# Kernel optimization log

Measured on AMD Instinct MI355X. Metric: run time of the kernel, lower is better.

## Reference

```python
import jax, jax.numpy as jnp
import numpy as np

N_HEADS = 32
N_KV_HEADS = 8
HEAD_DIM = 128
DIM = 4096
BSZ = 2
SEQLEN = 2048
ROPE_THETA = 500000.0


def setup_inputs() -> dict:
    key = jax.random.key(0)
    ks = jax.random.split(key, 6)
    s = 0.02
    x = jax.random.normal(ks[0], (BSZ, SEQLEN, DIM), dtype=jnp.float32)
    wq = jax.random.normal(ks[1], (N_HEADS * HEAD_DIM, DIM), dtype=jnp.float32) * s
    wk = jax.random.normal(ks[2], (N_KV_HEADS * HEAD_DIM, DIM), dtype=jnp.float32) * s
    wv = jax.random.normal(ks[3], (N_KV_HEADS * HEAD_DIM, DIM), dtype=jnp.float32) * s
    wo = jax.random.normal(ks[4], (DIM, N_HEADS * HEAD_DIM), dtype=jnp.float32) * s
    cache_k = jnp.zeros((BSZ, SEQLEN, N_KV_HEADS, HEAD_DIM), dtype=jnp.float32)
    cache_v = jnp.zeros((BSZ, SEQLEN, N_KV_HEADS, HEAD_DIM), dtype=jnp.float32)
    # rotary frequencies: freqs_cis[t, j] = exp(i * t * theta^(-2j/hd)); pass cos/sin parts
    inv = 1.0 / (ROPE_THETA ** (jnp.arange(0, HEAD_DIM, 2, dtype=jnp.float32) / HEAD_DIM))
    t = jnp.arange(SEQLEN, dtype=jnp.float32)
    ang = jnp.outer(t, inv)  # [S, hd/2]
    freqs_cos = jnp.cos(ang)
    freqs_sin = jnp.sin(ang)
    # causal additive mask
    mask = jnp.triu(jnp.full((SEQLEN, SEQLEN), -jnp.inf, dtype=jnp.float32), k=1)
    return {"x": x, "wq": wq, "wk": wk, "wv": wv, "wo": wo,
            "cache_k": cache_k, "cache_v": cache_v,
            "freqs_cos": freqs_cos, "freqs_sin": freqs_sin,
            "mask": mask, "start_pos": 0}


def _apply_rope(t, cos, sin):
    # t: [B, S, h, hd]; cos/sin: [S, hd/2]
    B, S, h, hd = t.shape
    tf = t.astype(jnp.float32).reshape(B, S, h, hd // 2, 2)
    a, b = tf[..., 0], tf[..., 1]
    c = cos[None, :, None, :]
    s = sin[None, :, None, :]
    out = jnp.stack([a * c - b * s, a * s + b * c], axis=-1)
    return out.reshape(B, S, h, hd).astype(t.dtype)


def reference(x, wq, wk, wv, wo, cache_k, cache_v, freqs_cos, freqs_sin, mask, start_pos):
    B, S, D = x.shape
    hd = HEAD_DIM
    n_rep = N_HEADS // N_KV_HEADS
    xq = (x @ wq.T).reshape(B, S, N_HEADS, hd)
    xk = (x @ wk.T).reshape(B, S, N_KV_HEADS, hd)
    xv = (x @ wv.T).reshape(B, S, N_KV_HEADS, hd)
    xq = _apply_rope(xq, freqs_cos, freqs_sin)
    xk = _apply_rope(xk, freqs_cos, freqs_sin)
    # KV cache write + slice
    cache_k = jax.lax.dynamic_update_slice(cache_k, xk, (0, start_pos, 0, 0))
    cache_v = jax.lax.dynamic_update_slice(cache_v, xv, (0, start_pos, 0, 0))
    kv_len = start_pos + S
    keys = cache_k[:B, :kv_len]    # [B, K, kvh, hd]
    values = cache_v[:B, :kv_len]
    # GQA: repeat kv heads
    keys = jnp.repeat(keys, n_rep, axis=2)     # [B, K, H, hd]
    values = jnp.repeat(values, n_rep, axis=2)
    q = xq.transpose(0, 2, 1, 3)       # [B, H, S, hd]
    k = keys.transpose(0, 2, 1, 3)     # [B, H, K, hd]
    v = values.transpose(0, 2, 1, 3)
    scores = jnp.einsum('bhqd,bhkd->bhqk', q, k) / jnp.sqrt(jnp.float32(hd))
    if mask is not None:
        scores = scores + mask[None, None, :, :]
    probs = jax.nn.softmax(scores.astype(jnp.float32), axis=-1).astype(q.dtype)
    out = jnp.einsum('bhqk,bhkd->bhqd', probs, v)
    out = out.transpose(0, 2, 1, 3).reshape(B, S, N_HEADS * hd)
    return out @ wo.T
```

## Files before the change

kernel.cpp:

```cpp
#include <hip/hip_runtime.h>
#include <hip/hip_bf16.h>
#include <math.h>

typedef __attribute__((ext_vector_type(8)))  __bf16 bfrag;
typedef __attribute__((ext_vector_type(4)))  float  f32x4;
typedef __attribute__((ext_vector_type(16))) float  f32x16;
typedef __attribute__((ext_vector_type(8)))  short  s16x8;
typedef __attribute__((ext_vector_type(4)))  short  s16x4;
typedef __attribute__((ext_vector_type(2)))  unsigned u32x2;
typedef __attribute__((ext_vector_type(4)))  unsigned u32x4;

__device__ __forceinline__ short f2bf(float f) {
  return (short)__builtin_bit_cast(unsigned short, (__bf16)f);
}
__device__ __forceinline__ float bf2f(short s) {
  return (float)__builtin_bit_cast(__bf16, (unsigned short)s);
}
__device__ __forceinline__ unsigned cvtpk(float lo, float hi_) {
  unsigned r;
  asm("v_cvt_pk_bf16_f32 %0, %1, %2" : "=v"(r) : "v"(lo), "v"(hi_));
  return r;
}
__device__ __forceinline__ void gll16(const void* g, void* l) {
  __builtin_amdgcn_global_load_lds((const __attribute__((address_space(1))) void*)g,
                                   (__attribute__((address_space(3))) void*)l, 16, 0, 0);
}

__global__ __launch_bounds__(256) void cvt_f32_bf16(const float* __restrict__ in,
                                                    short* __restrict__ out, int n4) {
  int i = blockIdx.x * 256 + threadIdx.x;
  if (i >= n4) return;
  f32x4 v = ((const f32x4*)in)[i];
  s16x4 o;
  o.x = f2bf(v.x); o.y = f2bf(v.y); o.z = f2bf(v.z); o.w = f2bf(v.w);
  ((s16x4*)out)[i] = o;
}

__global__ __launch_bounds__(256) void cvt4(const float* __restrict__ x,
                                            const float* __restrict__ wq,
                                            const float* __restrict__ wk,
                                            const float* __restrict__ wv,
                                            short* __restrict__ xb,
                                            short* __restrict__ wqb,
                                            short* __restrict__ wkb,
                                            short* __restrict__ wvb) {
  const int b = blockIdx.x;
  const float* in; short* out; int base;
  if (b < 16384)      { in = x;  out = xb;  base = 0; }
  else if (b < 32768) { in = wq; out = wqb; base = 16384 * 256; }
  else if (b < 36864) { in = wk; out = wkb; base = 32768 * 256; }
  else                { in = wv; out = wvb; base = 36864 * 256; }
  const int idx = b * 256 + threadIdx.x - base;
  f32x4 v = ((const f32x4*)in)[idx];
  s16x4 o;
  o.x = f2bf(v.x); o.y = f2bf(v.y); o.z = f2bf(v.z); o.w = f2bf(v.w);
  ((s16x4*)out)[idx] = o;
}

template<bool BF16OUT>
__global__ __launch_bounds__(512) void gemm128n(const short* __restrict__ A,
                                                const short* __restrict__ B,
                                                void* __restrict__ Cv,
                                                int M, int N, int K, int NBX) {
  __shared__ __align__(16) short As[2][128 * 64];
  __shared__ __align__(16) short Bs[2][256 * 64];
  const int tid = threadIdx.x, lane = tid & 63, wid = tid >> 6;
  const int lr = lane & 15, lg = lane >> 4;
  const int wm = wid >> 2, wn = wid & 3;
  const int nwg = gridDim.x, orig = blockIdx.x;
  const int qq = nwg >> 3, rr = nwg & 7, xc = orig & 7, o8 = orig >> 3;
  const int wg = (xc < rr ? xc * (qq + 1) : rr * (qq + 1) + (xc - rr) * qq) + o8;
  const int bm = (wg / NBX) << 7, bn = (wg % NBX) << 8;
  const int NT = K >> 6;
  const int r0 = tid >> 3;
  const int c0 = tid & 7;
  const int csrc = c0 ^ (r0 & 7);

#define STG(OP, OPs, boff, bb, hh, kt_)                                          \
  do {                                                                           \
    _Pragma("unroll")                                                            \
    for (int s = 0; s < 2; ++s)                                                  \
      gll16(OP + (size_t)(boff + (hh) * 128 + s * 64 + r0) * K + (kt_) * 64 + csrc * 8, \
            (char*)OPs[bb] + ((hh) * 128 + s * 64 + wid * 8) * 128);             \
  } while (0)

  int ch[2];
#pragma unroll
  for (int ks = 0; ks < 2; ++ks) ch[ks] = (((ks << 2) | lg) ^ (lr & 7)) << 4;
  const int aoff  = (wm * 64 + lr) * 128;
  const int boff2 = (wn * 32 + lr) * 128;

#define RD_A(dst, bb)                                                            \
  do {                                                                           \
    const char* ab = (const char*)As[bb] + aoff;                                 \
    _Pragma("unroll") for (int i = 0; i < 4; ++i)                                \
      _Pragma("unroll") for (int ks = 0; ks < 2; ++ks)                           \
        dst[i][ks] = *(const bfrag*)(ab + i * 2048 + ch[ks]);                    \
  } while (0)
#define RD_B(dst, bb, jh)                                                        \
  do {                                                                           \
    const char* bp = (const char*)Bs[bb] + boff2 + (jh) * 16384;                 \
    _Pragma("unroll") for (int j = 0; j < 2; ++j)                                \
      _Pragma("unroll") for (int ks = 0; ks < 2; ++ks)                           \
        dst[j][ks] = *(const bfrag*)(bp + j * 2048 + ch[ks]);                    \
  } while (0)
#define MFMA16(af, bf, jh)                                                       \
  do {                                                                           \
    __builtin_amdgcn_s_setprio(1);                                               \
    _Pragma("unroll") for (int ks = 0; ks < 2; ++ks)                             \
      _Pragma("unroll") for (int i = 0; i < 4; ++i)                              \
        _Pragma("unroll") for (int j = 0; j < 2; ++j)                            \
          acc[i][(jh) * 2 + j] = __builtin_amdgcn_mfma_f32_16x16x32_bf16(        \
              af[i][ks], bf[j][ks], acc[i][(jh) * 2 + j], 0, 0, 0);              \
    __builtin_amdgcn_s_setprio(0);                                               \
  } while (0)

  STG(A, As, bm, 0, 0, 0);
  STG(B, Bs, bn, 0, 0, 0);
  STG(B, Bs, bn, 0, 1, 0);
  if (NT > 1) {
    STG(A, As, bm, 1, 0, 1);
    STG(B, Bs, bn, 1, 0, 1);
    asm volatile("s_waitcnt vmcnt(4)" ::: "memory");
  } else {
    asm volatile("s_waitcnt vmcnt(0)" ::: "memory");
  }
  __builtin_amdgcn_s_barrier();
  __builtin_amdgcn_sched_barrier(0);

  f32x4 acc[4][4] = {};
  bfrag a_[4][2], b_lo[2][2], b_hi[2][2];

  for (int kt = 0; kt < NT; ++kt) {
    const int b = kt & 1;
    RD_A(a_, b);
    RD_B(b_lo, b, 0);
    if (kt + 1 < NT) STG(B, Bs, bn, b ^ 1, 1, kt + 1);
    MFMA16(a_, b_lo, 0);
    __builtin_amdgcn_s_barrier();
    __builtin_amdgcn_sched_barrier(0);
    RD_B(b_hi, b, 1);
    if (kt + 2 < NT) {
      STG(A, As, bm, b, 0, kt + 2);
      STG(B, Bs, bn, b, 0, kt + 2);
    }
    MFMA16(a_, b_hi, 1);
    if (kt + 1 < NT) {
      if (kt + 2 < NT) asm volatile("s_waitcnt vmcnt(4)" ::: "memory");
      else             asm volatile("s_waitcnt vmcnt(0)" ::: "memory");
      __builtin_amdgcn_s_barrier();
      __builtin_amdgcn_sched_barrier(0);
    }
  }
#undef STG
#undef RD_A
#undef RD_B
#undef MFMA16
  const int rb = bm + wm * 64 + lg * 4, cb = bn + wn * 32 + lr;
#pragma unroll
  for (int i = 0; i < 4; ++i)
#pragma unroll
    for (int jh = 0; jh < 2; ++jh)
#pragma unroll
      for (int j = 0; j < 2; ++j)
#pragma unroll
        for (int r = 0; r < 4; ++r) {
          size_t idx = (size_t)(rb + i * 16 + r) * N + (cb + jh * 128 + j * 16);
          if (BF16OUT) ((short*)Cv)[idx] = f2bf(acc[i][jh * 2 + j][r]);
          else         ((float*)Cv)[idx] = acc[i][jh * 2 + j][r];
        }
}

__global__ __launch_bounds__(256) void rope_k(short* __restrict__ qkv,
                                              const float* __restrict__ fcos,
                                              const float* __restrict__ fsin) {
  const int t = blockIdx.x;
  const int s = t & 2047;
  unsigned* row = (unsigned*)(qkv + (size_t)t * 6144);
  for (int p = threadIdx.x; p < 2560; p += 256) {
    const int h = p >> 6, i = p & 63;
    const int w = h * 64 + i;
    unsigned u = row[w];
    float a  = bf2f((short)(u & 0xffff));
    float b  = bf2f((short)(u >> 16));
    float c  = fcos[s * 64 + i], sn = fsin[s * 64 + i];
    float na = a * c - b * sn;
    float nb = a * sn + b * c;
    row[w] = ((unsigned)(unsigned short)f2bf(na)) |
             (((unsigned)(unsigned short)f2bf(nb)) << 16);
  }
}

__global__ __launch_bounds__(256) void vtrans(const short* __restrict__ qkv,
                                              short* __restrict__ vt) {
  const int sb = blockIdx.x, kvh = blockIdx.y, b = blockIdx.z;
  __shared__ short T[64][136];
  const int tid = threadIdx.x;
#pragma unroll
  for (int it = 0; it < 4; ++it) {
    int c = it * 256 + tid;
    int r = c >> 4, dc = c & 15;
    s16x8 v = *(const s16x8*)(qkv + (size_t)(b * 2048 + sb * 64 + r) * 6144
                              + 5120 + kvh * 128 + dc * 8);
    *(s16x8*)&T[r][dc * 8] = v;
  }
  __syncthreads();
#pragma unroll
  for (int it = 0; it < 4; ++it) {
    int c = it * 256 + tid;
    int d = c >> 3, sc = c & 7;
    s16x8 v;
#pragma unroll
    for (int j = 0; j < 8; ++j) v[j] = T[sc * 8 + j][d];
    *(s16x8*)(vt + (size_t)((b * 8 + kvh) * 128 + d) * 2048 + sb * 64 + sc * 8) = v;
  }
}

__global__ __launch_bounds__(512, 2) void fattn2(const short* __restrict__ qkv,
                                                 const short* __restrict__ vt,
                                                 short* __restrict__ ao) {
  const int qb = blockIdx.x, h = blockIdx.y, b = blockIdx.z;
  const int kvh = h >> 2;
  const int tid = threadIdx.x;
  const int lane = tid & 63, wid = tid >> 6;
  const int l31 = lane & 31, hi = lane >> 5;
  __shared__ __align__(16) short Ks[2][64 * 128];
  __shared__ __align__(16) short Vs[2][128 * 64];

  const int q0w   = qb * 256 + wid * 32;
  const int qg    = q0w + l31;
  const int tmaxw = q0w >> 6;
  const int NT    = 4 * qb + 4;

  bfrag qf[8];
  {
    const short* qp = qkv + (size_t)(b * 2048 + qg) * 6144 + h * 128 + hi * 8;
#pragma unroll
    for (int kk = 0; kk < 8; ++kk) qf[kk] = *(const bfrag*)(qp + kk * 16);
  }

  const int kr0 = tid >> 4, kcc = tid & 15;
  const int vd0 = tid >> 3, vkc = tid & 7;
  const int kro[2] = { kr0, kr0 + 32 };
  const int vdo[2] = { vd0, vd0 + 64 };
  int kldst[2], vldst[2];
#pragma unroll
  for (int i = 0; i < 2; ++i) {
    kldst[i] = (kro[i] * 256 + kcc * 16) ^ ((kro[i] & 7) << 4);
    vldst[i] = (vdo[i] * 128 + vkc * 16) ^ ((vdo[i] & 7) << 4);
  }
  const short* base_k = qkv + (size_t)(b * 2048) * 6144 + 4096 + kvh * 128;
  const short* base_v = vt + (size_t)((b * 8 + kvh) * 128) * 2048;

  {
    s16x8 kr_[2], vr_[2];
#pragma unroll
    for (int i = 0; i < 2; ++i) {
      kr_[i] = *(const s16x8*)(base_k + (size_t)kro[i] * 6144 + kcc * 8);
      vr_[i] = *(const s16x8*)(base_v + (size_t)vdo[i] * 2048 + vkc * 8);
    }
#pragma unroll
    for (int i = 0; i < 2; ++i) {
      *(s16x8*)((char*)Ks[0] + kldst[i]) = kr_[i];
      *(s16x8*)((char*)Vs[0] + vldst[i]) = vr_[i];
    }
  }
  __syncthreads();

  f32x16 o[4] = {};
  float m = -3.0e38f, l = 0.f;
  const float c0 = 0.08838834764831845f * 1.4426950408889634f;
  const int  sw = (l31 & 7) << 4;

  for (int t = 0; t < NT; ++t) {
    const int cur = t & 1;
    s16x8 kr_[2], vr_[2];
    const bool pf = (t + 1 < NT);
    if (pf) {
#pragma unroll
      for (int i = 0; i < 2; ++i) {
        kr_[i] = *(const s16x8*)(base_k + (size_t)((t + 1) * 64 + kro[i]) * 6144 + kcc * 8);
        vr_[i] = *(const s16x8*)(base_v + (size_t)vdo[i] * 2048 + (t + 1) * 64 + vkc * 8);
      }
    }
    if (t <= tmaxw) {
      f32x16 st[2] = {};
      {
        const char* kb = (const char*)Ks[cur] + l31 * 256;
        __builtin_amdgcn_s_setprio(1);
#pragma unroll
        for (int kk = 0; kk < 8; ++kk) {
          const int ko = (kk * 32 + hi * 16) ^ sw;
          bfrag kf0 = *(const bfrag*)(kb + ko);
          bfrag kf1 = *(const bfrag*)(kb + 8192 + ko);
          st[0] = __builtin_amdgcn_mfma_f32_32x32x16_bf16(kf0, qf[kk], st[0], 0, 0, 0);
          st[1] = __builtin_amdgcn_mfma_f32_32x32x16_bf16(kf1, qf[kk], st[1], 0, 0, 0);
        }
        __builtin_amdgcn_s_setprio(0);
      }
      if (t == tmaxw) {
        const int kb0 = t * 64 + 4 * hi;
#pragma unroll
        for (int kt = 0; kt < 2; ++kt)
#pragma unroll
          for (int r = 0; r < 16; ++r) {
            int k = kb0 + kt * 32 + (r & 3) + 8 * (r >> 2);
            if (k > qg) st[kt][r] = -3.0e38f;
          }
      }
      float mt = -3.0e38f;
#pragma unroll
      for (int kt = 0; kt < 2; ++kt)
#pragma unroll
        for (int r = 0; r < 16; ++r) mt = fmaxf(mt, st[kt][r]);
      mt = fmaxf(mt, __shfl_xor(mt, 32, 64));
      if (!__all((mt - m) * c0 <= 8.0f)) {
        float nm = fmaxf(m, mt);
        float fe = exp2f((m - nm) * c0);
        m = nm;
        l *= fe;
#pragma unroll
        for (int dt = 0; dt < 4; ++dt)
#pragma unroll
          for (int r = 0; r < 16; ++r) o[dt][r] *= fe;
      }
      const float mc = m * c0;
      float ps = 0.f;
#pragma unroll
      for (int kt = 0; kt < 2; ++kt)
#pragma unroll
        for (int r = 0; r < 16; ++r) {
          float p = exp2f(st[kt][r] * c0 - mc);
          st[kt][r] = p;
          ps += p;
        }
      ps += __shfl_xor(ps, 32, 64);
      l += ps;
      bfrag pfr[4];
#pragma unroll
      for (int kt = 0; kt < 2; ++kt) {
        u32x2 a0 = __builtin_amdgcn_permlane32_swap(cvtpk(st[kt][0],  st[kt][1]),
                                                    cvtpk(st[kt][4],  st[kt][5]),  0, 0);
        u32x2 a1 = __builtin_amdgcn_permlane32_swap(cvtpk(st[kt][2],  st[kt][3]),
                                                    cvtpk(st[kt][6],  st[kt][7]),  0, 0);
        u32x2 b0 = __builtin_amdgcn_permlane32_swap(cvtpk(st[kt][8],  st[kt][9]),
                                                    cvtpk(st[kt][12], st[kt][13]), 0, 0);
        u32x2 b1 = __builtin_amdgcn_permlane32_swap(cvtpk(st[kt][10], st[kt][11]),
                                                    cvtpk(st[kt][14], st[kt][15]), 0, 0);
        u32x4 w0 = { a0.x, a1.x, a0.y, a1.y };
        u32x4 w1 = { b0.x, b1.x, b0.y, b1.y };
        pfr[kt * 2]     = __builtin_bit_cast(bfrag, w0);
        pfr[kt * 2 + 1] = __builtin_bit_cast(bfrag, w1);
      }
      __builtin_amdgcn_s_setprio(1);
#pragma unroll
      for (int ks = 0; ks < 4; ++ks) {
        const char* vb = (const char*)Vs[cur] + l31 * 128 + ((ks * 32 + hi * 16) ^ sw);
#pragma unroll
        for (int dt = 0; dt < 4; ++dt) {
          bfrag vf = *(const bfrag*)(vb + dt * 4096);
          o[dt] = __builtin_amdgcn_mfma_f32_32x32x16_bf16(vf, pfr[ks], o[dt], 0, 0, 0);
        }
      }
      __builtin_amdgcn_s_setprio(0);
    }
    __syncthreads();
    if (pf) {
#pragma unroll
      for (int i = 0; i < 2; ++i) {
        *(s16x8*)((char*)Ks[cur ^ 1] + kldst[i]) = kr_[i];
        *(s16x8*)((char*)Vs[cur ^ 1] + vldst[i]) = vr_[i];
      }
    }
    __syncthreads();
  }
  const float linv = 1.f / l;
  short* aop = ao + (size_t)(b * 2048 + qg) * 4096 + h * 128 + 4 * hi;
#pragma unroll
  for (int dt = 0; dt < 4; ++dt)
#pragma unroll
    for (int r = 0; r < 16; ++r) {
      int d = dt * 32 + (r & 3) + 8 * (r >> 2);
      aop[d] = f2bf(o[dt][r] * linv);
    }
}

extern "C" void kernel_launch(void* const* d_in, const int* in_sizes, int n_in,
                              void* d_out, int out_size, void* d_ws, size_t ws_size,
                              hipStream_t stream) {
  const float* x  = (const float*)d_in[0];
  const float* wq = (const float*)d_in[1];
  const float* wk = (const float*)d_in[2];
  const float* wv = (const float*)d_in[3];
  const float* wo = (const float*)d_in[4];
  const float* fc = (const float*)d_in[7];
  const float* fs = (const float*)d_in[8];

  char* ws = (char*)d_ws;
  short* xb    = (short*)(ws);
  short* ao    = xb;
  short* wqkvb = (short*)(ws + 33554432ull);
  short* wob   = wqkvb;
  short* qkv   = (short*)(ws + 83886080ull);
  short* vt    = (short*)(ws + 134217728ull);

  cvt4<<<40960, 256, 0, stream>>>(x, wq, wk, wv,
                                  xb, wqkvb, wqkvb + 16777216, wqkvb + 20971520);
  gemm128n<true ><<<768, 512, 0, stream>>>(xb, wqkvb, qkv, 4096, 6144, 4096, 24);
  rope_k<<<4096, 256, 0, stream>>>(qkv, fc, fs);
  vtrans<<<dim3(32, 8, 2), 256, 0, stream>>>(qkv, vt);
  cvt_f32_bf16<<<16384, 256, 0, stream>>>(wo, wob, 4194304);
  fattn2<<<dim3(8, 32, 2), 512, 0, stream>>>(qkv, vt, ao);
  gemm128n<false><<<512, 512, 0, stream>>>(ao, wob, (float*)d_out, 4096, 4096, 4096, 16);
}
```

Measured before the change: 584.7 us.

## Switch GEMM to 32x32x16 MFMA with 2x2 wave tiles and simpler pipeline

Replaces the 16x16x32 MFMA GEMM inner loop with 32x32x16 MFMA instructions, so each wave computes a 64x64 sub-tile as 2x2 32x32 blocks instead of 64x32 split in two halves. The software pipeline is restructured: all of a stage's LDS fragments are read up front, then after a barrier the full next-next tile is prefetched, then all MFMAs run. The goal is fewer MFMA issues and better LDS reuse per fragment. The trade-off is an extra lgkmcnt wait and barrier per K step, which serialises LDS reads ahead of compute and loses the previous interleaving of loads and MFMAs.

```diff
diff --git a/kernel.cpp b/kernel.cpp
--- a/kernel.cpp
+++ b/kernel.cpp
@@ -58,14 +58,14 @@
 }
 
 template<bool BF16OUT>
-__global__ __launch_bounds__(512) void gemm128n(const short* __restrict__ A,
-                                                const short* __restrict__ B,
-                                                void* __restrict__ Cv,
-                                                int M, int N, int K, int NBX) {
+__global__ __launch_bounds__(512) void gemm32k(const short* __restrict__ A,
+                                               const short* __restrict__ B,
+                                               void* __restrict__ Cv,
+                                               int M, int N, int K, int NBX) {
   __shared__ __align__(16) short As[2][128 * 64];
   __shared__ __align__(16) short Bs[2][256 * 64];
   const int tid = threadIdx.x, lane = tid & 63, wid = tid >> 6;
-  const int lr = lane & 15, lg = lane >> 4;
+  const int l31 = lane & 31, hi = lane >> 5;
   const int wm = wid >> 2, wn = wid & 3;
   const int nwg = gridDim.x, orig = blockIdx.x;
   const int qq = nwg >> 3, rr = nwg & 7, xc = orig & 7, o8 = orig >> 3;
@@ -83,92 +83,82 @@
       gll16(OP + (size_t)(boff + (hh) * 128 + s * 64 + r0) * K + (kt_) * 64 + csrc * 8, \
             (char*)OPs[bb] + ((hh) * 128 + s * 64 + wid * 8) * 128);             \
   } while (0)
-
-  int ch[2];
-#pragma unroll
-  for (int ks = 0; ks < 2; ++ks) ch[ks] = (((ks << 2) | lg) ^ (lr & 7)) << 4;
-  const int aoff  = (wm * 64 + lr) * 128;
-  const int boff2 = (wn * 32 + lr) * 128;
-
-#define RD_A(dst, bb)                                                            \
+#define STG_TILE(bb, kt_)                                                        \
   do {                                                                           \
-    const char* ab = (const char*)As[bb] + aoff;                                 \
-    _Pragma("unroll") for (int i = 0; i < 4; ++i)                                \
-      _Pragma("unroll") for (int ks = 0; ks < 2; ++ks)                           \
-        dst[i][ks] = *(const bfrag*)(ab + i * 2048 + ch[ks]);                    \
+    STG(A, As, bm, bb, 0, kt_);                                                  \
+    STG(B, Bs, bn, bb, 0, kt_);                                                  \
+    STG(B, Bs, bn, bb, 1, kt_);                                                  \
   } while (0)
-#define RD_B(dst, bb, jh)                                                        \
-  do {                                                                           \
-    const char* bp = (const char*)Bs[bb] + boff2 + (jh) * 16384;                 \
-    _Pragma("unroll") for (int j = 0; j < 2; ++j)                                \
-      _Pragma("unroll") for (int ks = 0; ks < 2; ++ks)                           \
-        dst[j][ks] = *(const bfrag*)(bp + j * 2048 + ch[ks]);                    \
-  } while (0)
-#define MFMA16(af, bf, jh)                                                       \
-  do {                                                                           \
-    __builtin_amdgcn_s_setprio(1);                                               \
-    _Pragma("unroll") for (int ks = 0; ks < 2; ++ks)                             \
-      _Pragma("unroll") for (int i = 0; i < 4; ++i)                              \
-        _Pragma("unroll") for (int j = 0; j < 2; ++j)                            \
-          acc[i][(jh) * 2 + j] = __builtin_amdgcn_mfma_f32_16x16x32_bf16(        \
-              af[i][ks], bf[j][ks], acc[i][(jh) * 2 + j], 0, 0, 0);              \
-    __builtin_amdgcn_s_setprio(0);                                               \
-  } while (0)
-
-  STG(A, As, bm, 0, 0, 0);
-  STG(B, Bs, bn, 0, 0, 0);
-  STG(B, Bs, bn, 0, 1, 0);
+
+  const int swz = (l31 & 7) << 4;
+  int ko[4];
+#pragma unroll
+  for (int ks = 0; ks < 4; ++ks) ko[ks] = (ks * 32 + hi * 16) ^ swz;
+  const int aoff = (wm * 64 + l31) * 128;
+  const int boff = (wn * 64 + l31) * 128;
+
+  STG_TILE(0, 0);
   if (NT > 1) {
-    STG(A, As, bm, 1, 0, 1);
-    STG(B, Bs, bn, 1, 0, 1);
-    asm volatile("s_waitcnt vmcnt(4)" ::: "memory");
+    STG_TILE(1, 1);
+    asm volatile("s_waitcnt vmcnt(6)" ::: "memory");
   } else {
     asm volatile("s_waitcnt vmcnt(0)" ::: "memory");
   }
   __builtin_amdgcn_s_barrier();
   __builtin_amdgcn_sched_barrier(0);
 
-  f32x4 acc[4][4] = {};
-  bfrag a_[4][2], b_lo[2][2], b_hi[2][2];
+  f32x16 acc[2][2] = {};
+  bfrag a_[2][4], b_[2][4];
 
   for (int kt = 0; kt < NT; ++kt) {
-    const int b = kt & 1;
-    RD_A(a_, b);
-    RD_B(b_lo, b, 0);
-    if (kt + 1 < NT) STG(B, Bs, bn, b ^ 1, 1, kt + 1);
-    MFMA16(a_, b_lo, 0);
+    const int p = kt & 1;
+    const char* Ab = (const char*)As[p] + aoff;
+    const char* Bb = (const char*)Bs[p] + boff;
+#pragma unroll
+    for (int mt = 0; mt < 2; ++mt)
+#pragma unroll
+      for (int ks = 0; ks < 4; ++ks)
+        a_[mt][ks] = *(const bfrag*)(Ab + mt * 4096 + ko[ks]);
+#pragma unroll
+    for (int nt = 0; nt < 2; ++nt)
+#pragma unroll
+      for (int ks = 0; ks < 4; ++ks)
+        b_[nt][ks] = *(const bfrag*)(Bb + nt * 4096 + ko[ks]);
+    asm volatile("s_waitcnt lgkmcnt(0)" ::: "memory");
     __builtin_amdgcn_s_barrier();
     __builtin_amdgcn_sched_barrier(0);
-    RD_B(b_hi, b, 1);
-    if (kt + 2 < NT) {
-      STG(A, As, bm, b, 0, kt + 2);
-      STG(B, Bs, bn, b, 0, kt + 2);
-    }
-    MFMA16(a_, b_hi, 1);
+    if (kt + 2 < NT) STG_TILE(p, kt + 2);
+    __builtin_amdgcn_s_setprio(1);
+#pragma unroll
+    for (int ks = 0; ks < 4; ++ks)
+#pragma unroll
+      for (int mt = 0; mt < 2; ++mt)
+#pragma unroll
+        for (int nt = 0; nt < 2; ++nt)
+          acc[mt][nt] = __builtin_amdgcn_mfma_f32_32x32x16_bf16(
+              a_[mt][ks], b_[nt][ks], acc[mt][nt], 0, 0, 0);
+    __builtin_amdgcn_s_setprio(0);
     if (kt + 1 < NT) {
-      if (kt + 2 < NT) asm volatile("s_waitcnt vmcnt(4)" ::: "memory");
+      if (kt + 2 < NT) asm volatile("s_waitcnt vmcnt(6)" ::: "memory");
       else             asm volatile("s_waitcnt vmcnt(0)" ::: "memory");
       __builtin_amdgcn_s_barrier();
       __builtin_amdgcn_sched_barrier(0);
     }
   }
 #undef STG
-#undef RD_A
-#undef RD_B
-#undef MFMA16
-  const int rb = bm + wm * 64 + lg * 4, cb = bn + wn * 32 + lr;
-#pragma unroll
-  for (int i = 0; i < 4; ++i)
-#pragma unroll
-    for (int jh = 0; jh < 2; ++jh)
-#pragma unroll
-      for (int j = 0; j < 2; ++j)
-#pragma unroll
-        for (int r = 0; r < 4; ++r) {
-          size_t idx = (size_t)(rb + i * 16 + r) * N + (cb + jh * 128 + j * 16);
-          if (BF16OUT) ((short*)Cv)[idx] = f2bf(acc[i][jh * 2 + j][r]);
-          else         ((float*)Cv)[idx] = acc[i][jh * 2 + j][r];
-        }
+#undef STG_TILE
+  const int rb = bm + wm * 64 + 4 * hi, cb = bn + wn * 64 + l31;
+#pragma unroll
+  for (int mt = 0; mt < 2; ++mt)
+#pragma unroll
+    for (int nt = 0; nt < 2; ++nt)
+#pragma unroll
+      for (int r = 0; r < 16; ++r) {
+        const int row = rb + mt * 32 + (r & 3) + 8 * (r >> 2);
+        size_t idx = (size_t)row * N + (cb + nt * 32);
+        if (BF16OUT) ((short*)Cv)[idx] = f2bf(acc[mt][nt][r]);
+        else         ((float*)Cv)[idx] = acc[mt][nt][r];
+      }
 }
 
 __global__ __launch_bounds__(256) void rope_k(short* __restrict__ qkv,
@@ -406,10 +396,10 @@
 
   cvt4<<<40960, 256, 0, stream>>>(x, wq, wk, wv,
                                   xb, wqkvb, wqkvb + 16777216, wqkvb + 20971520);
-  gemm128n<true ><<<768, 512, 0, stream>>>(xb, wqkvb, qkv, 4096, 6144, 4096, 24);
+  gemm32k<true ><<<768, 512, 0, stream>>>(xb, wqkvb, qkv, 4096, 6144, 4096, 24);
   rope_k<<<4096, 256, 0, stream>>>(qkv, fc, fs);
   vtrans<<<dim3(32, 8, 2), 256, 0, stream>>>(qkv, vt);
   cvt_f32_bf16<<<16384, 256, 0, stream>>>(wo, wob, 4194304);
   fattn2<<<dim3(8, 32, 2), 512, 0, stream>>>(qkv, vt, ao);
-  gemm128n<false><<<512, 512, 0, stream>>>(ao, wob, (float*)d_out, 4096, 4096, 4096, 16);
-}
+  gemm32k<false><<<512, 512, 0, stream>>>(ao, wob, (float*)d_out, 4096, 4096, 4096, 16);
+}
```

Measured after the change: 693.5 us. 18.6% more time.
